# Kernel tuning notes

Measured on AMD Instinct MI355X. Metric: run time of the kernel, lower is better.

Reference implementation:

```python
import jax, jax.numpy as jnp
import numpy as np

N_NODES = 100000
N_EDGES = 800000
NODE_F = 32
EDGE_F = 16
HID = 128
EPS = 1e-5


def _bn(h, g, b):
    # BatchNorm1d in training mode: biased batch stats over dim 0
    m = h.mean(axis=0)
    v = jnp.mean((h - m) ** 2, axis=0)
    return (h - m) * jax.lax.rsqrt(v + EPS) * g + b


def _sage(x, src, dst, Wl, bl, Wr):
    # PyG SAGEConv (mean aggr): lin_l(mean_{j->i} x_j) + lin_r(x_i)
    s = jax.ops.segment_sum(x[src], dst, num_segments=N_NODES)
    cnt = jax.ops.segment_sum(jnp.ones((src.shape[0], 1), x.dtype), dst, num_segments=N_NODES)
    mean = s / jnp.maximum(cnt, 1.0)
    return mean @ Wl + bl + x @ Wr


def setup_inputs() -> dict:
    key = jax.random.key(0)
    ks = jax.random.split(key, 32)

    def lin(k, fi, fo):
        return jax.random.normal(k, (fi, fo), jnp.float32) / np.sqrt(fi)

    inp = {
        'x': jax.random.normal(ks[0], (N_NODES, NODE_F), jnp.float32),
        'edge_index': jax.random.randint(ks[1], (2, N_EDGES), 0, N_NODES),
        'edge_attr': jax.random.normal(ks[2], (N_EDGES, EDGE_F), jnp.float32),
        'edge_source': jax.random.randint(ks[3], (N_EDGES,), 0, N_NODES),
        'edge_target': jax.random.randint(ks[4], (N_EDGES,), 0, N_NODES),
        'W1l': lin(ks[5], NODE_F, HID), 'b1': jnp.zeros((HID,), jnp.float32), 'W1r': lin(ks[6], NODE_F, HID),
        'W2l': lin(ks[7], HID, HID), 'b2': jnp.zeros((HID,), jnp.float32), 'W2r': lin(ks[8], HID, HID),
        'bn1_g': jnp.ones((HID,), jnp.float32), 'bn1_b': jnp.zeros((HID,), jnp.float32),
        'bn2_g': jnp.ones((HID,), jnp.float32), 'bn2_b': jnp.zeros((HID,), jnp.float32),
        'We': lin(ks[9], EDGE_F, HID), 'be': jnp.zeros((HID,), jnp.float32),
        'bne_g': jnp.ones((HID,), jnp.float32), 'bne_b': jnp.zeros((HID,), jnp.float32),
        'Wm1': lin(ks[10], 3 * HID, HID), 'bm1': jnp.zeros((HID,), jnp.float32),
        'bnm_g': jnp.ones((HID,), jnp.float32), 'bnm_b': jnp.zeros((HID,), jnp.float32),
        'Wm2': lin(ks[11], HID, HID // 2), 'bm2': jnp.zeros((HID // 2,), jnp.float32),
        'Wm3': lin(ks[12], HID // 2, 1), 'bm3': jnp.zeros((1,), jnp.float32),
    }
    return inp


def reference(x, edge_index, edge_attr, edge_source, edge_target,
              W1l, b1, W1r, W2l, b2, W2r, bn1_g, bn1_b, bn2_g, bn2_b,
              We, be, bne_g, bne_b, Wm1, bm1, bnm_g, bnm_b, Wm2, bm2, Wm3, bm3):
    src, dst = edge_index[0], edge_index[1]
    h = jax.nn.relu(_bn(_sage(x, src, dst, W1l, b1, W1r), bn1_g, bn1_b))  # dropout = identity (eval)
    h = jax.nn.relu(_bn(_sage(h, src, dst, W2l, b2, W2r), bn2_g, bn2_b))
    ef = _bn(jax.nn.relu(edge_attr @ We + be), bne_g, bne_b)  # Linear->ReLU->BN->Dropout(id)
    z = jnp.concatenate([h[edge_source], h[edge_target], ef], axis=1)  # [E, 3*HID]
    z = _bn(jax.nn.relu(z @ Wm1 + bm1), bnm_g, bnm_b)
    z = jax.nn.relu(z @ Wm2 + bm2)
    return (z @ Wm3 + bm3).squeeze(-1)
```

## Files before the change

### kernel.cpp

```cpp
#include <hip/hip_runtime.h>
#include <hip/hip_bf16.h>

#define NN 100000
#define NE 800000
#define SCAN_NB 98

typedef __attribute__((ext_vector_type(8))) short bf16x8;
typedef __attribute__((ext_vector_type(4))) float f32x4;

__device__ __forceinline__ short f2b(float f) {
    unsigned u = __float_as_uint(f);
    unsigned r = (u + 0x7fffu + ((u >> 16) & 1u)) >> 16;
    return (short)r;
}
__device__ __forceinline__ float b2f(short s) {
    return __uint_as_float(((unsigned)(unsigned short)s) << 16);
}

__global__ __launch_bounds__(256) void k_hist(const int* __restrict__ ei, int* __restrict__ deg)
{
    int e = blockIdx.x * 256 + threadIdx.x;
    if (e < NE) atomicAdd(&deg[ei[NE + e]], 1);
}

__global__ __launch_bounds__(1024) void k_scan_a(const int* __restrict__ deg,
    int* __restrict__ tmp, int* __restrict__ bsum)
{
    __shared__ int sh[1024];
    int t = threadIdx.x, b = blockIdx.x;
    int idx = b * 1024 + t;
    int v = (idx < NN) ? deg[idx] : 0;
    sh[t] = v;
    __syncthreads();
    for (int ofs = 1; ofs < 1024; ofs <<= 1) {
        int u = (t >= ofs) ? sh[t - ofs] : 0;
        __syncthreads();
        sh[t] += u;
        __syncthreads();
    }
    if (idx < NN) tmp[idx] = sh[t] - v;
    if (t == 1023) bsum[b] = sh[1023];
}

__global__ void k_scan_b(const int* __restrict__ bsum, int* __restrict__ boff,
    int* __restrict__ rowptr)
{
    if (threadIdx.x == 0) {
        int acc = 0;
        for (int i = 0; i < SCAN_NB; i++) { boff[i] = acc; acc += bsum[i]; }
        rowptr[NN] = acc;
    }
}

__global__ __launch_bounds__(1024) void k_scan_c(const int* __restrict__ tmp,
    const int* __restrict__ boff, int* __restrict__ rowptr, int* __restrict__ wp)
{
    int b = blockIdx.x, t = threadIdx.x;
    int idx = b * 1024 + t;
    if (idx < NN) {
        int v = boff[b] + tmp[idx];
        rowptr[idx] = v; wp[idx] = v;
    }
}

__global__ __launch_bounds__(256) void k_scatter(const int* __restrict__ ei,
    int* __restrict__ wp, int* __restrict__ elist)
{
    int e = blockIdx.x * 256 + threadIdx.x;
    if (e < NE) {
        int d = ei[NE + e];
        int pos = atomicAdd(&wp[d], 1);
        elist[pos] = ei[e];
    }
}

__global__ __launch_bounds__(256) void k_gagg1(const float* __restrict__ x,
    const int* __restrict__ rowptr, const int* __restrict__ elist, float* __restrict__ meanX)
{
    int n = blockIdx.x * 8 + (threadIdx.x >> 5);
    int j = threadIdx.x & 31;
    int b = rowptr[n], e = rowptr[n + 1];
    float acc = 0.f;
    for (int i = b; i < e; i++) {
        int s = elist[i];
        acc += x[(size_t)s * 32 + j];
    }
    float inv = (e > b) ? 1.0f / (float)(e - b) : 1.0f;
    meanX[(size_t)n * 32 + j] = acc * inv;
}

__global__ __launch_bounds__(256) void k_gagg2(const short* __restrict__ h1b,
    const int* __restrict__ rowptr, const int* __restrict__ elist,
    const float* __restrict__ ssum, const float* __restrict__ ssq,
    const float* __restrict__ g, const float* __restrict__ bb, short* __restrict__ m2b)
{
    __shared__ float sS[128], sH[128];
    int tid = threadIdx.x;
    if (tid < 128) {
        float m = ssum[tid] / (float)NN;
        float var = ssq[tid] / (float)NN - m * m;
        float rs = rsqrtf(var + 1e-5f);
        float sc = g[tid] * rs;
        sS[tid] = sc; sH[tid] = bb[tid] - m * sc;
    }
    __syncthreads();
    int n = blockIdx.x * 8 + (tid >> 5);
    int c0 = (tid & 31) * 4;
    float sc[4], sh[4];
    #pragma unroll
    for (int i = 0; i < 4; i++) { sc[i] = sS[c0 + i]; sh[i] = sH[c0 + i]; }
    int b = rowptr[n], e = rowptr[n + 1];
    float acc[4] = {0.f, 0.f, 0.f, 0.f};
    for (int i = b; i < e; i++) {
        int s = elist[i];
        ushort4 u = *(const ushort4*)(h1b + (size_t)s * 128 + c0);
        acc[0] += fmaxf(b2f((short)u.x) * sc[0] + sh[0], 0.f);
        acc[1] += fmaxf(b2f((short)u.y) * sc[1] + sh[1], 0.f);
        acc[2] += fmaxf(b2f((short)u.z) * sc[2] + sh[2], 0.f);
        acc[3] += fmaxf(b2f((short)u.w) * sc[3] + sh[3], 0.f);
    }
    float inv = (e > b) ? 1.0f / (float)(e - b) : 1.0f;
    ushort4 o;
    o.x = (unsigned short)f2b(acc[0] * inv);
    o.y = (unsigned short)f2b(acc[1] * inv);
    o.z = (unsigned short)f2b(acc[2] * inv);
    o.w = (unsigned short)f2b(acc[3] * inv);
    *(ushort4*)(m2b + (size_t)n * 128 + c0) = o;
}

__global__ __launch_bounds__(256) void k_node_l1(
    const float* __restrict__ meanX, const float* __restrict__ x,
    const float* __restrict__ Wl, const float* __restrict__ Wr,
    const float* __restrict__ bias,
    short* __restrict__ outp, float* __restrict__ ssum, float* __restrict__ ssq)
{
    __shared__ __align__(16) float sWl[32][128];
    __shared__ __align__(16) float sWr[32][128];
    __shared__ __align__(16) float sA[32][36];
    __shared__ __align__(16) float sB[32][36];
    __shared__ float red[2][128], red2[2][128];
    int tid = threadIdx.x;
    int j = tid & 127, rg = tid >> 7;
    int r0 = blockIdx.x * 32;

    for (int f = tid * 4; f < 4096; f += 1024) {
        *(float4*)((float*)sWl + f) = *(const float4*)(Wl + f);
        *(float4*)((float*)sWr + f) = *(const float4*)(Wr + f);
    }
    {
        int r = tid >> 3, c = (tid & 7) * 4;
        *(float4*)(&sA[r][c]) = *(const float4*)(meanX + (size_t)(r0 + r) * 32 + c);
        *(float4*)(&sB[r][c]) = *(const float4*)(x + (size_t)(r0 + r) * 32 + c);
    }
    __syncthreads();

    float acc[16];
    #pragma unroll
    for (int r = 0; r < 16; r++) acc[r] = 0.0f;
    int rb = rg * 16;
    #pragma unroll
    for (int kq = 0; kq < 8; kq++) {
        int k = kq * 4;
        float wl0 = sWl[k][j], wl1 = sWl[k+1][j], wl2 = sWl[k+2][j], wl3 = sWl[k+3][j];
        float wr0 = sWr[k][j], wr1 = sWr[k+1][j], wr2 = sWr[k+2][j], wr3 = sWr[k+3][j];
        #pragma unroll
        for (int r = 0; r < 16; r++) {
            float4 a = *(float4*)(&sA[rb + r][k]);
            float4 b = *(float4*)(&sB[rb + r][k]);
            acc[r] += a.x*wl0 + a.y*wl1 + a.z*wl2 + a.w*wl3
                    + b.x*wr0 + b.y*wr1 + b.z*wr2 + b.w*wr3;
        }
    }
    float bj = bias[j];
    float s1 = 0.0f, s2 = 0.0f;
    #pragma unroll
    for (int r = 0; r < 16; r++) {
        float v = acc[r] + bj;
        outp[(size_t)(r0 + rb + r) * 128 + j] = f2b(v);
        s1 += v; s2 += v * v;
    }
    red[rg][j] = s1; red2[rg][j] = s2;
    __syncthreads();
    if (rg == 0) {
        atomicAdd(&ssum[j], red[0][j] + red[1][j]);
        atomicAdd(&ssq[j],  red2[0][j] + red2[1][j]);
    }
}

__global__ __launch_bounds__(256) void k_node_l2m(
    const short* __restrict__ m2b, const short* __restrict__ h1b,
    const float* __restrict__ s1sum, const float* __restrict__ s1sq,
    const float* __restrict__ g1, const float* __restrict__ b1b,
    const short* __restrict__ W2cT, const float* __restrict__ bias,
    short* __restrict__ h2b, float* __restrict__ ssum, float* __restrict__ ssq)
{
    __shared__ __align__(16) short sK[32][264];
    __shared__ float sRed[2][128];
    __shared__ float sS[128], sH[128];
    const int tid = threadIdx.x;
    const int wave = tid >> 6, lane = tid & 63, quad = lane >> 4, ln = lane & 15;
    const int waveM = wave >> 1, waveN = wave & 1;
    const int colbase = 64 * waveN, row16 = 16 * waveM;
    if (tid < 128) {
        float m = s1sum[tid] / (float)NN;
        float var = s1sq[tid] / (float)NN - m * m;
        float rs = rsqrtf(var + 1e-5f);
        float sc = g1[tid] * rs;
        sS[tid] = sc; sH[tid] = b1b[tid] - m * sc;
        sRed[0][tid] = 0.f; sRed[1][tid] = 0.f;
    }

    bf16x8 bW[4][8];
    #pragma unroll
    for (int nt = 0; nt < 4; nt++)
        #pragma unroll
        for (int kk = 0; kk < 8; kk++)
            bW[nt][kk] = *(const bf16x8*)(W2cT + (size_t)(colbase + nt * 16 + ln) * 256 + kk * 32 + quad * 8);
    float bc[4];
    #pragma unroll
    for (int nt = 0; nt < 4; nt++) bc[nt] = bias[colbase + nt * 16 + ln];

    float s1[4] = {0,0,0,0}, s2[4] = {0,0,0,0};
    f32x4 zero = {0.f, 0.f, 0.f, 0.f};
    __syncthreads();

    for (int t = blockIdx.x; t < NN / 32; t += gridDim.x) {
        int r0 = t * 32;
        __syncthreads();
        {
            int r = tid >> 3, seg = tid & 7;
            if (seg < 4) {
                const bf16x8* src = (const bf16x8*)(m2b + (size_t)(r0 + r) * 128 + seg * 32);
                bf16x8* dst = (bf16x8*)(&sK[r][seg * 32]);
                dst[0] = src[0]; dst[1] = src[1]; dst[2] = src[2]; dst[3] = src[3];
            } else {
                int c0 = (seg - 4) * 32;
                const short* src = h1b + (size_t)(r0 + r) * 128 + c0;
                short tmp[32];
                #pragma unroll
                for (int i = 0; i < 32; i++)
                    tmp[i] = f2b(fmaxf(b2f(src[i]) * sS[c0 + i] + sH[c0 + i], 0.f));
                bf16x8* dst = (bf16x8*)(&sK[r][128 + c0]);
                dst[0] = *(bf16x8*)(tmp); dst[1] = *(bf16x8*)(tmp + 8);
                dst[2] = *(bf16x8*)(tmp + 16); dst[3] = *(bf16x8*)(tmp + 24);
            }
        }
        __syncthreads();
        f32x4 acc[4] = {zero, zero, zero, zero};
        #pragma unroll
        for (int kk = 0; kk < 8; kk++) {
            bf16x8 a = *(const bf16x8*)(&sK[row16 + ln][kk * 32 + quad * 8]);
            #pragma unroll
            for (int nt = 0; nt < 4; nt++)
                acc[nt] = __builtin_amdgcn_mfma_f32_16x16x32_bf16(a, bW[nt][kk], acc[nt], 0, 0, 0);
        }
        #pragma unroll
        for (int nt = 0; nt < 4; nt++) {
            int col = colbase + nt * 16 + ln;
            #pragma unroll
            for (int r = 0; r < 4; r++) {
                float v = acc[nt][r] + bc[nt];
                h2b[(size_t)(r0 + row16 + quad * 4 + r) * 128 + col] = f2b(v);
                s1[nt] += v; s2[nt] += v * v;
            }
        }
    }
    #pragma unroll
    for (int nt = 0; nt < 4; nt++) {
        float a1 = s1[nt], a2 = s2[nt];
        a1 += __shfl_down(a1, 32); a1 += __shfl_down(a1, 16);
        a2 += __shfl_down(a2, 32); a2 += __shfl_down(a2, 16);
        if (quad == 0) {
            atomicAdd(&sRed[0][colbase + nt * 16 + ln], a1);
            atomicAdd(&sRed[1][colbase + nt * 16 + ln], a2);
        }
    }
    __syncthreads();
    if (tid < 128) {
        atomicAdd(&ssum[tid], sRed[0][tid]);
        atomicAdd(&ssq[tid],  sRed[1][tid]);
    }
}

__global__ void k_prep(const float* __restrict__ We, const float* __restrict__ Wm1,
                       const float* __restrict__ W2l, const float* __restrict__ W2r,
                       short* __restrict__ WteT, short* __restrict__ WmsT,
                       short* __restrict__ WmdT, short* __restrict__ W2cT)
{
    int j = threadIdx.x;
    int b = blockIdx.x;
    if (b == 0) {
        for (int k = 0; k < 32; k++)
            WteT[j * 32 + k] = (k < 16) ? f2b(We[k * 128 + j]) : (short)0;
    } else if (b == 1) {
        for (int k = 0; k < 128; k++) WmsT[j * 128 + k] = f2b(Wm1[k * 128 + j]);
    } else if (b == 2) {
        for (int k = 0; k < 128; k++) WmdT[j * 128 + k] = f2b(Wm1[(128 + k) * 128 + j]);
    } else if (b == 3) {
        for (int k = 0; k < 128; k++) W2cT[j * 256 + k] = f2b(W2l[k * 128 + j]);
    } else {
        for (int k = 0; k < 128; k++) W2cT[j * 256 + 128 + k] = f2b(W2r[k * 128 + j]);
    }
}

__global__ void k_fold_e(const float* __restrict__ ssum, const float* __restrict__ ssq,
    const float* __restrict__ g, const float* __restrict__ b,
    const float* __restrict__ Wm1, const float* __restrict__ bm1,
    short* __restrict__ W1pT, float* __restrict__ bm1p)
{
    __shared__ float sa[128], sc[128];
    int tid = threadIdx.x;
    float m = ssum[tid] / (float)NE;
    float var = ssq[tid] / (float)NE - m * m;
    float rs = rsqrtf(var + 1e-5f);
    float a = g[tid] * rs;
    sa[tid] = a; sc[tid] = b[tid] - m * a;
    __syncthreads();
    float acc = bm1[tid];
    for (int k = 0; k < 128; k++) {
        float w = Wm1[(256 + k) * 128 + tid];
        W1pT[tid * 128 + k] = f2b(sa[k] * w);
        acc += sc[k] * w;
    }
    bm1p[tid] = acc;
}

__global__ void k_fold_m(const float* __restrict__ ssum, const float* __restrict__ ssq,
    const float* __restrict__ g, const float* __restrict__ b,
    const float* __restrict__ Wm2, const float* __restrict__ bm2,
    short* __restrict__ W2pT, float* __restrict__ b2p)
{
    __shared__ float sa[128], sc[128];
    int tid = threadIdx.x;
    float m = ssum[tid] / (float)NE;
    float var = ssq[tid] / (float)NE - m * m;
    float rs = rsqrtf(var + 1e-5f);
    float a = g[tid] * rs;
    sa[tid] = a; sc[tid] = b[tid] - m * a;
    __syncthreads();
    if (tid < 64) {
        float acc = bm2[tid];
        for (int k = 0; k < 128; k++) {
            float w = Wm2[k * 64 + tid];
            W2pT[tid * 128 + k] = f2b(sa[k] * w);
            acc += sc[k] * w;
        }
        b2p[tid] = acc;
    }
}

__global__ __launch_bounds__(256) void k_proj2(
    const short* __restrict__ h2b,
    const float* __restrict__ s2sum, const float* __restrict__ s2sq,
    const float* __restrict__ g2, const float* __restrict__ b2b,
    const short* __restrict__ WsT, const short* __restrict__ WdT,
    short* __restrict__ Cs, short* __restrict__ Cd)
{
    __shared__ __align__(16) short sA[32][136];
    __shared__ float sS[128], sH[128];
    const int tid = threadIdx.x;
    const int wave = tid >> 6, lane = tid & 63, quad = lane >> 4, ln = lane & 15;
    const int waveM = wave >> 1, waveN = wave & 1;
    const int colbase = 64 * waveN, row16 = 16 * waveM;
    if (tid < 128) {
        float m = s2sum[tid] / (float)NN;
        float var = s2sq[tid] / (float)NN - m * m;
        float rs = rsqrtf(var + 1e-5f);
        float sc = g2[tid] * rs;
        sS[tid] = sc; sH[tid] = b2b[tid] - m * sc;
    }
    bf16x8 bWs[4][4], bWd[4][4];
    #pragma unroll
    for (int nt = 0; nt < 4; nt++)
        #pragma unroll
        for (int kk = 0; kk < 4; kk++) {
            bWs[nt][kk] = *(const bf16x8*)(WsT + (colbase + nt * 16 + ln) * 128 + kk * 32 + quad * 8);
            bWd[nt][kk] = *(const bf16x8*)(WdT + (colbase + nt * 16 + ln) * 128 + kk * 32 + quad * 8);
        }
    f32x4 zero = {0.f, 0.f, 0.f, 0.f};
    __syncthreads();
    for (int t = blockIdx.x; t < NN / 32; t += gridDim.x) {
        int r0 = t * 32;
        __syncthreads();
        {
            int r = tid >> 3, c0 = (tid & 7) * 16;
            const short* p = h2b + (size_t)(r0 + r) * 128 + c0;
            short tmp[16];
            #pragma unroll
            for (int i = 0; i < 16; i++)
                tmp[i] = f2b(fmaxf(b2f(p[i]) * sS[c0 + i] + sH[c0 + i], 0.f));
            *(bf16x8*)(&sA[r][c0])     = *(bf16x8*)tmp;
            *(bf16x8*)(&sA[r][c0 + 8]) = *(bf16x8*)(tmp + 8);
        }
        __syncthreads();
        f32x4 accS[4] = {zero, zero, zero, zero};
        f32x4 accD[4] = {zero, zero, zero, zero};
        #pragma unroll
        for (int kk = 0; kk < 4; kk++) {
            bf16x8 a = *(const bf16x8*)(&sA[row16 + ln][kk * 32 + quad * 8]);
            #pragma unroll
            for (int nt = 0; nt < 4; nt++) {
                accS[nt] = __builtin_amdgcn_mfma_f32_16x16x32_bf16(a, bWs[nt][kk], accS[nt], 0, 0, 0);
                accD[nt] = __builtin_amdgcn_mfma_f32_16x16x32_bf16(a, bWd[nt][kk], accD[nt], 0, 0, 0);
            }
        }
        #pragma unroll
        for (int nt = 0; nt < 4; nt++) {
            int col = colbase + nt * 16 + ln;
            #pragma unroll
            for (int r = 0; r < 4; r++) {
                size_t idx = (size_t)(r0 + row16 + quad * 4 + r) * 128 + col;
                Cs[idx] = f2b(accS[nt][r]);
                Cd[idx] = f2b(accD[nt][r]);
            }
        }
    }
}

template<int MODE>
__global__ __launch_bounds__(256) void k_edge_mfma(
    const float* __restrict__ ea, short* __restrict__ ea_bf,
    const short* __restrict__ WteT, const float* __restrict__ be,
    const short* __restrict__ W1pT, const float* __restrict__ bm1p,
    const short* __restrict__ hs, const short* __restrict__ hd,
    const int* __restrict__ esrc, const int* __restrict__ etgt,
    const short* __restrict__ W2pT, const float* __restrict__ b2p,
    const float* __restrict__ Wm3, const float* __restrict__ bm3,
    float* __restrict__ ssum, float* __restrict__ ssq,
    float* __restrict__ outp)
{
    __shared__ __align__(16) short sT[32][136];
    __shared__ float sRed[2][128];
    __shared__ __align__(16) float sG[32][132];
    __shared__ __align__(16) short sW2[64][136];
    __shared__ float sZ[32][69];
    __shared__ float sW3[64];

    const int tid = threadIdx.x;
    const int wave = tid >> 6, lane = tid & 63;
    const int quad = lane >> 4, ln = lane & 15;
    const int waveM = wave >> 1, waveN = wave & 1;
    const int colbase = 64 * waveN, row16 = 16 * waveM;

    if (MODE < 2) {
        if (tid < 128) { sRed[0][tid] = 0.f; sRed[1][tid] = 0.f; }
    }
    if (MODE == 2) {
        int q = tid >> 2, kb = (tid & 3) * 32;
        const bf16x8* src = (const bf16x8*)(W2pT + q * 128 + kb);
        bf16x8* dst = (bf16x8*)(&sW2[q][kb]);
        dst[0] = src[0]; dst[1] = src[1]; dst[2] = src[2]; dst[3] = src[3];
        if (tid < 64) sW3[tid] = Wm3[tid];
    }

    bf16x8 bWe[4], bW1[4][4];
    #pragma unroll
    for (int nt = 0; nt < 4; nt++) {
        bWe[nt] = *(const bf16x8*)(WteT + (colbase + nt * 16 + ln) * 32 + quad * 8);
        if (MODE >= 1) {
            #pragma unroll
            for (int kk = 0; kk < 4; kk++)
                bW1[nt][kk] = *(const bf16x8*)(W1pT + (colbase + nt * 16 + ln) * 128 + kk * 32 + quad * 8);
        }
    }
    float bec[4], bmc[4];
    #pragma unroll
    for (int nt = 0; nt < 4; nt++) {
        bec[nt] = be[colbase + nt * 16 + ln];
        bmc[nt] = (MODE >= 1) ? bm1p[colbase + nt * 16 + ln] : 0.f;
    }
    float b2c[2] = {0.f, 0.f};
    if (MODE == 2) { b2c[0] = b2p[32 * waveN + ln]; b2c[1] = b2p[32 * waveN + 16 + ln]; }
    float bm3v = (MODE == 2) ? bm3[0] : 0.f;

    const int g_er = tid >> 3, g_cb = (tid & 7) * 16;

    float s1[4] = {0,0,0,0}, s2[4] = {0,0,0,0};
    f32x4 zero = {0.f, 0.f, 0.f, 0.f};
    __syncthreads();

    for (int t = blockIdx.x; t < NE / 32; t += gridDim.x) {
        const int e0 = t * 32;

        bf16x8 ga0, ga1, gb0, gb1;
        if (MODE >= 1) {
            int es_ = esrc[e0 + g_er], et_ = etgt[e0 + g_er];
            const short* ps = hs + (size_t)es_ * 128 + g_cb;
            const short* pd = hd + (size_t)et_ * 128 + g_cb;
            ga0 = *(const bf16x8*)ps;      ga1 = *(const bf16x8*)(ps + 8);
            gb0 = *(const bf16x8*)pd;      gb1 = *(const bf16x8*)(pd + 8);
        }

        bf16x8 aE;
        #pragma unroll
        for (int i = 0; i < 8; i++) aE[i] = 0;
        if (MODE == 0) {
            if (quad < 2) {
                const float* p = ea + (size_t)(e0 + row16 + ln) * 16 + quad * 8;
                float4 f0 = *(const float4*)p, f1 = *(const float4*)(p + 4);
                aE[0]=f2b(f0.x); aE[1]=f2b(f0.y); aE[2]=f2b(f0.z); aE[3]=f2b(f0.w);
                aE[4]=f2b(f1.x); aE[5]=f2b(f1.y); aE[6]=f2b(f1.z); aE[7]=f2b(f1.w);
                if (waveN == 0)
                    *(bf16x8*)(ea_bf + (size_t)(e0 + row16 + ln) * 16 + quad * 8) = aE;
            }
        } else {
            if (quad < 2)
                aE = *(const bf16x8*)(ea_bf + (size_t)(e0 + row16 + ln) * 16 + quad * 8);
        }
        f32x4 tacc[4];
        #pragma unroll
        for (int nt = 0; nt < 4; nt++)
            tacc[nt] = __builtin_amdgcn_mfma_f32_16x16x32_bf16(aE, bWe[nt], tacc[nt] = zero, 0, 0, 0);

        if (MODE == 0) {
            #pragma unroll
            for (int nt = 0; nt < 4; nt++)
                #pragma unroll
                for (int r = 0; r < 4; r++) {
                    float v = fmaxf(tacc[nt][r] + bec[nt], 0.f);
                    s1[nt] += v; s2[nt] += v * v;
                }
            continue;
        }

        __syncthreads();
        #pragma unroll
        for (int nt = 0; nt < 4; nt++) {
            int col = colbase + nt * 16 + ln;
            #pragma unroll
            for (int r = 0; r < 4; r++)
                sT[row16 + quad * 4 + r][col] = f2b(fmaxf(tacc[nt][r] + bec[nt], 0.f));
        }
        {
            float tf[16];
            #pragma unroll
            for (int i = 0; i < 8; i++) {
                tf[i]     = b2f(ga0[i]) + b2f(gb0[i]);
                tf[8 + i] = b2f(ga1[i]) + b2f(gb1[i]);
            }
            #pragma unroll
            for (int q4 = 0; q4 < 4; q4++)
                *(float4*)(&sG[g_er][g_cb + q4 * 4]) = *(float4*)(tf + q4 * 4);
        }
        __syncthreads();

        f32x4 uacc[4] = {zero, zero, zero, zero};
        #pragma unroll
        for (int kk = 0; kk < 4; kk++) {
            bf16x8 aU = *(const bf16x8*)(&sT[row16 + ln][kk * 32 + quad * 8]);
            #pragma unroll
            for (int nt = 0; nt < 4; nt++)
                uacc[nt] = __builtin_amdgcn_mfma_f32_16x16x32_bf16(aU, bW1[nt][kk], uacc[nt], 0, 0, 0);
        }

        if (MODE == 1) {
            #pragma unroll
            for (int nt = 0; nt < 4; nt++) {
                int col = colbase + nt * 16 + ln;
                #pragma unroll
                for (int r = 0; r < 4; r++) {
                    float v = uacc[nt][r] + bmc[nt] + sG[row16 + quad * 4 + r][col];
                    v = fmaxf(v, 0.f);
                    s1[nt] += v; s2[nt] += v * v;
                }
            }
        } else {
            __syncthreads();
            #pragma unroll
            for (int nt = 0; nt < 4; nt++) {
                int col = colbase + nt * 16 + ln;
                #pragma unroll
                for (int r = 0; r < 4; r++) {
                    float v = uacc[nt][r] + bmc[nt] + sG[row16 + quad * 4 + r][col];
                    sT[row16 + quad * 4 + r][col] = f2b(fmaxf(v, 0.f));
                }
            }
            __syncthreads();
            f32x4 vacc[2] = {zero, zero};
            #pragma unroll
            for (int kk = 0; kk < 4; kk++) {
                bf16x8 aV = *(const bf16x8*)(&sT[row16 + ln][kk * 32 + quad * 8]);
                #pragma unroll
                for (int n2 = 0; n2 < 2; n2++) {
                    bf16x8 bV = *(const bf16x8*)(&sW2[32 * waveN + n2 * 16 + ln][kk * 32 + quad * 8]);
                    vacc[n2] = __builtin_amdgcn_mfma_f32_16x16x32_bf16(aV, bV, vacc[n2], 0, 0, 0);
                }
            }
            #pragma unroll
            for (int n2 = 0; n2 < 2; n2++) {
                int col2 = 32 * waveN + n2 * 16 + ln;
                #pragma unroll
                for (int r = 0; r < 4; r++)
                    sZ[row16 + quad * 4 + r][col2] = fmaxf(vacc[n2][r] + b2c[n2], 0.f);
            }
            __syncthreads();
            if (wave == 0) {
                int rw = lane & 31, half = lane >> 5;
                float o = 0.f;
                #pragma unroll 8
                for (int k2 = 0; k2 < 32; k2++)
                    o += sZ[rw][half * 32 + k2] * sW3[half * 32 + k2];
                o += __shfl_down(o, 32);
                if (lane < 32) outp[e0 + rw] = o + bm3v;
            }
        }
    }

    if (MODE < 2) {
        #pragma unroll
        for (int nt = 0; nt < 4; nt++) {
            float a1 = s1[nt], a2 = s2[nt];
            a1 += __shfl_down(a1, 32); a1 += __shfl_down(a1, 16);
            a2 += __shfl_down(a2, 32); a2 += __shfl_down(a2, 16);
            if (quad == 0) {
                atomicAdd(&sRed[0][colbase + nt * 16 + ln], a1);
                atomicAdd(&sRed[1][colbase + nt * 16 + ln], a2);
            }
        }
        __syncthreads();
        if (tid < 128) {
            atomicAdd(&ssum[tid], sRed[0][tid]);
            atomicAdd(&ssq[tid],  sRed[1][tid]);
        }
    }
}

extern "C" void kernel_launch(void* const* d_in, const int* in_sizes, int n_in,
                              void* d_out, int out_size, void* d_ws, size_t ws_size,
                              hipStream_t stream) {
    const float* x     = (const float*)d_in[0];
    const int*   ei    = (const int*)  d_in[1];
    const float* eattr = (const float*)d_in[2];
    const int*   esrc  = (const int*)  d_in[3];
    const int*   etgt  = (const int*)  d_in[4];
    const float* W1l = (const float*)d_in[5];  const float* b1 = (const float*)d_in[6];
    const float* W1r = (const float*)d_in[7];
    const float* W2l = (const float*)d_in[8];  const float* b2 = (const float*)d_in[9];
    const float* W2r = (const float*)d_in[10];
    const float* bn1_g = (const float*)d_in[11]; const float* bn1_b = (const float*)d_in[12];
    const float* bn2_g = (const float*)d_in[13]; const float* bn2_b = (const float*)d_in[14];
    const float* We  = (const float*)d_in[15]; const float* be  = (const float*)d_in[16];
    const float* bne_g = (const float*)d_in[17]; const float* bne_b = (const float*)d_in[18];
    const float* Wm1 = (const float*)d_in[19]; const float* bm1 = (const float*)d_in[20];
    const float* bnm_g = (const float*)d_in[21]; const float* bnm_b = (const float*)d_in[22];
    const float* Wm2 = (const float*)d_in[23]; const float* bm2 = (const float*)d_in[24];
    const float* Wm3 = (const float*)d_in[25]; const float* bm3 = (const float*)d_in[26];
    float* out = (float*)d_out;

    char* base = (char*)d_ws;
    size_t o = 0;
    auto A = [&](size_t bytes) { char* p = base + o; o = (o + bytes + 255) & ~(size_t)255; return p; };
    short* hsb   = (short*)A((size_t)NN * 128 * 2);
    short* hdb   = (short*)A((size_t)NN * 128 * 2);
    short* ea_bf = (short*)A((size_t)NE * 16 * 2);
    int*   deg   = (int*)  A((size_t)NN * 4);
    int*   rowptr= (int*)  A((size_t)(NN + 1) * 4);
    int*   wp    = (int*)  A((size_t)NN * 4);
    int*   elist = (int*)  A((size_t)NE * 4);
    float* st    = (float*)A(1024 * 4);
    int*   bsum  = (int*)  A(SCAN_NB * 4);
    int*   boff  = (int*)  A(SCAN_NB * 4);
    float* bm1p  = (float*)A(512); float* b2p = (float*)A(256);
    short* WteT  = (short*)A(128 * 32 * 2);
    short* W1pT  = (short*)A(128 * 128 * 2);
    short* WmsT  = (short*)A(128 * 128 * 2);
    short* WmdT  = (short*)A(128 * 128 * 2);
    short* W2pT  = (short*)A(64 * 128 * 2);
    short* W2cT  = (short*)A(128 * 256 * 2);
    float* meanX = (float*)A((size_t)NN * 32 * 4);
    short* h1b   = (short*)A((size_t)NN * 128 * 2);
    short* m2b   = (short*)A((size_t)NN * 128 * 2);
    short* h2b   = (short*)A((size_t)NN * 128 * 2);
    int*   stmp  = (int*)meanX;

    hipMemsetAsync(deg, 0, (size_t)NN * 4, stream);
    hipMemsetAsync(st, 0, 1024 * 4, stream);

    k_prep<<<5, 128, 0, stream>>>(We, Wm1, W2l, W2r, WteT, WmsT, WmdT, W2cT);
    k_hist<<<(NE + 255) / 256, 256, 0, stream>>>(ei, deg);
    k_scan_a<<<SCAN_NB, 1024, 0, stream>>>(deg, stmp, bsum);
    k_scan_b<<<1, 64, 0, stream>>>(bsum, boff, rowptr);
    k_scan_c<<<SCAN_NB, 1024, 0, stream>>>(stmp, boff, rowptr, wp);
    k_scatter<<<(NE + 255) / 256, 256, 0, stream>>>(ei, wp, elist);

    k_edge_mfma<0><<<1024, 256, 0, stream>>>(eattr, ea_bf, WteT, be, W1pT, bm1p, hsb, hdb,
        esrc, etgt, W2pT, b2p, Wm3, bm3, st + 512, st + 640, out);
    k_fold_e<<<1, 128, 0, stream>>>(st + 512, st + 640, bne_g, bne_b, Wm1, bm1, W1pT, bm1p);

    k_gagg1<<<NN / 8, 256, 0, stream>>>(x, rowptr, elist, meanX);
    k_node_l1<<<NN / 32, 256, 0, stream>>>(meanX, x, W1l, W1r, b1, h1b, st + 0, st + 128);

    k_gagg2<<<NN / 8, 256, 0, stream>>>(h1b, rowptr, elist, st + 0, st + 128, bn1_g, bn1_b, m2b);
    k_node_l2m<<<640, 256, 0, stream>>>(m2b, h1b, st + 0, st + 128, bn1_g, bn1_b,
                                        W2cT, b2, h2b, st + 256, st + 384);

    k_proj2<<<640, 256, 0, stream>>>(h2b, st + 256, st + 384, bn2_g, bn2_b, WmsT, WmdT, hsb, hdb);

    k_edge_mfma<1><<<2048, 256, 0, stream>>>(eattr, ea_bf, WteT, be, W1pT, bm1p, hsb, hdb,
        esrc, etgt, W2pT, b2p, Wm3, bm3, st + 768, st + 896, out);
    k_fold_m<<<1, 128, 0, stream>>>(st + 768, st + 896, bnm_g, bnm_b, Wm2, bm2, W2pT, b2p);

    k_edge_mfma<2><<<2048, 256, 0, stream>>>(eattr, ea_bf, WteT, be, W1pT, bm1p, hsb, hdb,
        esrc, etgt, W2pT, b2p, Wm3, bm3, nullptr, nullptr, out);
}
```

Baseline: 876.7 us.

## Shrink edge kernel LDS via per-mode pool, keep W2 in registers, shuffle final dot

Replaces fixed shared arrays with a per-MODE sized LDS pool so MODE 0 uses almost no LDS and modes 1/2 use less, which allows more resident blocks. W2 tiles are now held in registers instead of being staged in LDS. The final 64-to-1 projection is done with in-wave shuffles instead of an sZ staging buffer read by a single wave. One barrier is dropped in MODE 2. The cost is more VGPRs for the bW2 fragments, and the missing barrier relies on the later barriers to protect reuse of sT and sG across iterations.

```diff
diff --git a/kernel.cpp b/kernel.cpp
--- a/kernel.cpp
+++ b/kernel.cpp
@@ -429,12 +429,12 @@
     float* __restrict__ ssum, float* __restrict__ ssq,
     float* __restrict__ outp)
 {
-    __shared__ __align__(16) short sT[32][136];
-    __shared__ float sRed[2][128];
-    __shared__ __align__(16) float sG[32][132];
-    __shared__ __align__(16) short sW2[64][136];
-    __shared__ float sZ[32][69];
-    __shared__ float sW3[64];
+    constexpr int POOL = (MODE == 0) ? 1024 : (MODE == 1 ? 25600 + 1024 : 25600 + 256);
+    __shared__ __align__(16) char pool[POOL];
+    short (*sT)[136] = (short(*)[136])pool;
+    float (*sG)[132] = (float(*)[132])(pool + 8704);
+    float* sRed = (float*)((MODE == 0) ? (char*)pool : pool + 25600);
+    float (*sP)[32] = (float(*)[32])(pool + 25600);
 
     const int tid = threadIdx.x;
     const int wave = tid >> 6, lane = tid & 63;
@@ -443,14 +443,7 @@
     const int colbase = 64 * waveN, row16 = 16 * waveM;
 
     if (MODE < 2) {
-        if (tid < 128) { sRed[0][tid] = 0.f; sRed[1][tid] = 0.f; }
-    }
-    if (MODE == 2) {
-        int q = tid >> 2, kb = (tid & 3) * 32;
-        const bf16x8* src = (const bf16x8*)(W2pT + q * 128 + kb);
-        bf16x8* dst = (bf16x8*)(&sW2[q][kb]);
-        dst[0] = src[0]; dst[1] = src[1]; dst[2] = src[2]; dst[3] = src[3];
-        if (tid < 64) sW3[tid] = Wm3[tid];
+        if (tid < 128) { sRed[tid] = 0.f; sRed[128 + tid] = 0.f; }
     }
 
     bf16x8 bWe[4], bW1[4][4];
@@ -469,8 +462,19 @@
         bec[nt] = be[colbase + nt * 16 + ln];
         bmc[nt] = (MODE >= 1) ? bm1p[colbase + nt * 16 + ln] : 0.f;
     }
-    float b2c[2] = {0.f, 0.f};
-    if (MODE == 2) { b2c[0] = b2p[32 * waveN + ln]; b2c[1] = b2p[32 * waveN + 16 + ln]; }
+    bf16x8 bW2[2][4];
+    float b2c[2] = {0.f, 0.f}, w3c[2] = {0.f, 0.f};
+    if (MODE == 2) {
+        #pragma unroll
+        for (int n2 = 0; n2 < 2; n2++) {
+            int col2 = 32 * waveN + n2 * 16 + ln;
+            b2c[n2] = b2p[col2];
+            w3c[n2] = Wm3[col2];
+            #pragma unroll
+            for (int kk = 0; kk < 4; kk++)
+                bW2[n2][kk] = *(const bf16x8*)(W2pT + col2 * 128 + kk * 32 + quad * 8);
+        }
+    }
     float bm3v = (MODE == 2) ? bm3[0] : 0.f;
 
     const int g_er = tid >> 3, g_cb = (tid & 7) * 16;
@@ -510,7 +514,7 @@
         f32x4 tacc[4];
         #pragma unroll
         for (int nt = 0; nt < 4; nt++)
-            tacc[nt] = __builtin_amdgcn_mfma_f32_16x16x32_bf16(aE, bWe[nt], tacc[nt] = zero, 0, 0, 0);
+            tacc[nt] = __builtin_amdgcn_mfma_f32_16x16x32_bf16(aE, bWe[nt], zero, 0, 0, 0);
 
         if (MODE == 0) {
             #pragma unroll
@@ -523,7 +527,7 @@
             continue;
         }
 
-        __syncthreads();
+        if (MODE == 1) __syncthreads();
         #pragma unroll
         for (int nt = 0; nt < 4; nt++) {
             int col = colbase + nt * 16 + ln;
@@ -581,28 +585,19 @@
             for (int kk = 0; kk < 4; kk++) {
                 bf16x8 aV = *(const bf16x8*)(&sT[row16 + ln][kk * 32 + quad * 8]);
                 #pragma unroll
-                for (int n2 = 0; n2 < 2; n2++) {
-                    bf16x8 bV = *(const bf16x8*)(&sW2[32 * waveN + n2 * 16 + ln][kk * 32 + quad * 8]);
-                    vacc[n2] = __builtin_amdgcn_mfma_f32_16x16x32_bf16(aV, bV, vacc[n2], 0, 0, 0);
-                }
-            }
-            #pragma unroll
-            for (int n2 = 0; n2 < 2; n2++) {
-                int col2 = 32 * waveN + n2 * 16 + ln;
-                #pragma unroll
-                for (int r = 0; r < 4; r++)
-                    sZ[row16 + quad * 4 + r][col2] = fmaxf(vacc[n2][r] + b2c[n2], 0.f);
+                for (int n2 = 0; n2 < 2; n2++)
+                    vacc[n2] = __builtin_amdgcn_mfma_f32_16x16x32_bf16(aV, bW2[n2][kk], vacc[n2], 0, 0, 0);
+            }
+            #pragma unroll
+            for (int r = 0; r < 4; r++) {
+                float p = fmaxf(vacc[0][r] + b2c[0], 0.f) * w3c[0]
+                        + fmaxf(vacc[1][r] + b2c[1], 0.f) * w3c[1];
+                p += __shfl_xor(p, 1); p += __shfl_xor(p, 2);
+                p += __shfl_xor(p, 4); p += __shfl_xor(p, 8);
+                if (ln == 0) sP[waveN][row16 + quad * 4 + r] = p;
             }
             __syncthreads();
-            if (wave == 0) {
-                int rw = lane & 31, half = lane >> 5;
-                float o = 0.f;
-                #pragma unroll 8
-                for (int k2 = 0; k2 < 32; k2++)
-                    o += sZ[rw][half * 32 + k2] * sW3[half * 32 + k2];
-                o += __shfl_down(o, 32);
-                if (lane < 32) outp[e0 + rw] = o + bm3v;
-            }
+            if (tid < 32) outp[e0 + tid] = sP[0][tid] + sP[1][tid] + bm3v;
         }
     }
 
@@ -613,14 +608,14 @@
             a1 += __shfl_down(a1, 32); a1 += __shfl_down(a1, 16);
             a2 += __shfl_down(a2, 32); a2 += __shfl_down(a2, 16);
             if (quad == 0) {
-                atomicAdd(&sRed[0][colbase + nt * 16 + ln], a1);
-                atomicAdd(&sRed[1][colbase + nt * 16 + ln], a2);
+                atomicAdd(&sRed[colbase + nt * 16 + ln], a1);
+                atomicAdd(&sRed[128 + colbase + nt * 16 + ln], a2);
             }
         }
         __syncthreads();
         if (tid < 128) {
-            atomicAdd(&ssum[tid], sRed[0][tid]);
-            atomicAdd(&ssq[tid],  sRed[1][tid]);
+            atomicAdd(&ssum[tid], sRed[tid]);
+            atomicAdd(&ssq[tid],  sRed[128 + tid]);
         }
     }
 }
```

Result: slower. 912.2 us (+4.0%).

## Store MLP hidden activations to skip recomputation in final edge pass

Applied to the files above, without the earlier changes.

When workspace is large enough, the first MLP edge pass writes the post-ReLU hidden activations as bf16 to a buffer that reuses the node-stage scratch region. A new mode-3 pass then reads them back and runs only the second and third layers, avoiding a second round of endpoint gathers and the first-layer GEMM. The first pass also software-prefetches the next tile's gathered rows, and the source/target projection kernel is split into two launches with half the register weights each. This trades 200MB of extra writes and reads for the recomputation, and it depends on the workspace size.

```diff
diff --git a/kernel.cpp b/kernel.cpp
--- a/kernel.cpp
+++ b/kernel.cpp
@@ -349,12 +349,11 @@
     }
 }
 
-__global__ __launch_bounds__(256) void k_proj2(
+__global__ __launch_bounds__(256) void k_proj_mfma(
     const short* __restrict__ h2b,
     const float* __restrict__ s2sum, const float* __restrict__ s2sq,
     const float* __restrict__ g2, const float* __restrict__ b2b,
-    const short* __restrict__ WsT, const short* __restrict__ WdT,
-    short* __restrict__ Cs, short* __restrict__ Cd)
+    const short* __restrict__ WT, short* __restrict__ C)
 {
     __shared__ __align__(16) short sA[32][136];
     __shared__ float sS[128], sH[128];
@@ -369,14 +368,12 @@
         float sc = g2[tid] * rs;
         sS[tid] = sc; sH[tid] = b2b[tid] - m * sc;
     }
-    bf16x8 bWs[4][4], bWd[4][4];
+    bf16x8 bW[4][4];
     #pragma unroll
     for (int nt = 0; nt < 4; nt++)
         #pragma unroll
-        for (int kk = 0; kk < 4; kk++) {
-            bWs[nt][kk] = *(const bf16x8*)(WsT + (colbase + nt * 16 + ln) * 128 + kk * 32 + quad * 8);
-            bWd[nt][kk] = *(const bf16x8*)(WdT + (colbase + nt * 16 + ln) * 128 + kk * 32 + quad * 8);
-        }
+        for (int kk = 0; kk < 4; kk++)
+            bW[nt][kk] = *(const bf16x8*)(WT + (colbase + nt * 16 + ln) * 128 + kk * 32 + quad * 8);
     f32x4 zero = {0.f, 0.f, 0.f, 0.f};
     __syncthreads();
     for (int t = blockIdx.x; t < NN / 32; t += gridDim.x) {
@@ -393,31 +390,25 @@
             *(bf16x8*)(&sA[r][c0 + 8]) = *(bf16x8*)(tmp + 8);
         }
         __syncthreads();
-        f32x4 accS[4] = {zero, zero, zero, zero};
-        f32x4 accD[4] = {zero, zero, zero, zero};
+        f32x4 acc[4] = {zero, zero, zero, zero};
         #pragma unroll
         for (int kk = 0; kk < 4; kk++) {
             bf16x8 a = *(const bf16x8*)(&sA[row16 + ln][kk * 32 + quad * 8]);
             #pragma unroll
-            for (int nt = 0; nt < 4; nt++) {
-                accS[nt] = __builtin_amdgcn_mfma_f32_16x16x32_bf16(a, bWs[nt][kk], accS[nt], 0, 0, 0);
-                accD[nt] = __builtin_amdgcn_mfma_f32_16x16x32_bf16(a, bWd[nt][kk], accD[nt], 0, 0, 0);
-            }
+            for (int nt = 0; nt < 4; nt++)
+                acc[nt] = __builtin_amdgcn_mfma_f32_16x16x32_bf16(a, bW[nt][kk], acc[nt], 0, 0, 0);
         }
         #pragma unroll
         for (int nt = 0; nt < 4; nt++) {
             int col = colbase + nt * 16 + ln;
             #pragma unroll
-            for (int r = 0; r < 4; r++) {
-                size_t idx = (size_t)(r0 + row16 + quad * 4 + r) * 128 + col;
-                Cs[idx] = f2b(accS[nt][r]);
-                Cd[idx] = f2b(accD[nt][r]);
-            }
-        }
-    }
-}
-
-template<int MODE>
+            for (int r = 0; r < 4; r++)
+                C[(size_t)(r0 + row16 + quad * 4 + r) * 128 + col] = f2b(acc[nt][r]);
+        }
+    }
+}
+
+template<int MODE, bool STOREV = false>
 __global__ __launch_bounds__(256) void k_edge_mfma(
     const float* __restrict__ ea, short* __restrict__ ea_bf,
     const short* __restrict__ WteT, const float* __restrict__ be,
@@ -427,7 +418,7 @@
     const short* __restrict__ W2pT, const float* __restrict__ b2p,
     const float* __restrict__ Wm3, const float* __restrict__ bm3,
     float* __restrict__ ssum, float* __restrict__ ssq,
-    float* __restrict__ outp)
+    short* __restrict__ vbuf, float* __restrict__ outp)
 {
     __shared__ __align__(16) short sT[32][136];
     __shared__ float sRed[2][128];
@@ -445,7 +436,7 @@
     if (MODE < 2) {
         if (tid < 128) { sRed[0][tid] = 0.f; sRed[1][tid] = 0.f; }
     }
-    if (MODE == 2) {
+    if (MODE >= 2) {
         int q = tid >> 2, kb = (tid & 3) * 32;
         const bf16x8* src = (const bf16x8*)(W2pT + q * 128 + kb);
         bf16x8* dst = (bf16x8*)(&sW2[q][kb]);
@@ -454,41 +445,90 @@
     }
 
     bf16x8 bWe[4], bW1[4][4];
+    if (MODE <= 2) {
+        #pragma unroll
+        for (int nt = 0; nt < 4; nt++) {
+            bWe[nt] = *(const bf16x8*)(WteT + (colbase + nt * 16 + ln) * 32 + quad * 8);
+            if (MODE >= 1) {
+                #pragma unroll
+                for (int kk = 0; kk < 4; kk++)
+                    bW1[nt][kk] = *(const bf16x8*)(W1pT + (colbase + nt * 16 + ln) * 128 + kk * 32 + quad * 8);
+            }
+        }
+    }
+    float bec[4], bmc[4];
     #pragma unroll
     for (int nt = 0; nt < 4; nt++) {
-        bWe[nt] = *(const bf16x8*)(WteT + (colbase + nt * 16 + ln) * 32 + quad * 8);
-        if (MODE >= 1) {
-            #pragma unroll
-            for (int kk = 0; kk < 4; kk++)
-                bW1[nt][kk] = *(const bf16x8*)(W1pT + (colbase + nt * 16 + ln) * 128 + kk * 32 + quad * 8);
-        }
-    }
-    float bec[4], bmc[4];
-    #pragma unroll
-    for (int nt = 0; nt < 4; nt++) {
-        bec[nt] = be[colbase + nt * 16 + ln];
-        bmc[nt] = (MODE >= 1) ? bm1p[colbase + nt * 16 + ln] : 0.f;
+        bec[nt] = (MODE <= 2) ? be[colbase + nt * 16 + ln] : 0.f;
+        bmc[nt] = (MODE == 1 || MODE == 2) ? bm1p[colbase + nt * 16 + ln] : 0.f;
     }
     float b2c[2] = {0.f, 0.f};
-    if (MODE == 2) { b2c[0] = b2p[32 * waveN + ln]; b2c[1] = b2p[32 * waveN + 16 + ln]; }
-    float bm3v = (MODE == 2) ? bm3[0] : 0.f;
+    if (MODE >= 2) { b2c[0] = b2p[32 * waveN + ln]; b2c[1] = b2p[32 * waveN + 16 + ln]; }
+    float bm3v = (MODE >= 2) ? bm3[0] : 0.f;
 
     const int g_er = tid >> 3, g_cb = (tid & 7) * 16;
+    const int NT = NE / 32;
+
+    bf16x8 ga0, ga1, gb0, gb1;
+    if (MODE == 1 && blockIdx.x < NT) {
+        int es0 = esrc[blockIdx.x * 32 + g_er], et0 = etgt[blockIdx.x * 32 + g_er];
+        const short* ps = hs + (size_t)es0 * 128 + g_cb;
+        const short* pd = hd + (size_t)et0 * 128 + g_cb;
+        ga0 = *(const bf16x8*)ps; ga1 = *(const bf16x8*)(ps + 8);
+        gb0 = *(const bf16x8*)pd; gb1 = *(const bf16x8*)(pd + 8);
+    }
 
     float s1[4] = {0,0,0,0}, s2[4] = {0,0,0,0};
     f32x4 zero = {0.f, 0.f, 0.f, 0.f};
     __syncthreads();
 
-    for (int t = blockIdx.x; t < NE / 32; t += gridDim.x) {
+    for (int t = blockIdx.x; t < NT; t += gridDim.x) {
         const int e0 = t * 32;
 
-        bf16x8 ga0, ga1, gb0, gb1;
-        if (MODE >= 1) {
+        if (MODE == 3) {
+            f32x4 vacc[2] = {zero, zero};
+            #pragma unroll
+            for (int kk = 0; kk < 4; kk++) {
+                bf16x8 aV = *(const bf16x8*)(vbuf + (size_t)(e0 + row16 + ln) * 128 + kk * 32 + quad * 8);
+                #pragma unroll
+                for (int n2 = 0; n2 < 2; n2++) {
+                    bf16x8 bV = *(const bf16x8*)(&sW2[32 * waveN + n2 * 16 + ln][kk * 32 + quad * 8]);
+                    vacc[n2] = __builtin_amdgcn_mfma_f32_16x16x32_bf16(aV, bV, vacc[n2], 0, 0, 0);
+                }
+            }
+            __syncthreads();
+            #pragma unroll
+            for (int n2 = 0; n2 < 2; n2++) {
+                int col2 = 32 * waveN + n2 * 16 + ln;
+                #pragma unroll
+                for (int r = 0; r < 4; r++)
+                    sZ[row16 + quad * 4 + r][col2] = fmaxf(vacc[n2][r] + b2c[n2], 0.f);
+            }
+            __syncthreads();
+            if (wave == 0) {
+                int rw = lane & 31, half = lane >> 5;
+                float o = 0.f;
+                #pragma unroll 8
+                for (int k2 = 0; k2 < 32; k2++)
+                    o += sZ[rw][half * 32 + k2] * sW3[half * 32 + k2];
+                o += __shfl_down(o, 32);
+                if (lane < 32) outp[e0 + rw] = o + bm3v;
+            }
+            continue;
+        }
+
+        int tn = t + gridDim.x;
+        int es_n = 0, et_n = 0;
+        if (MODE == 1 && tn < NT) {
+            es_n = esrc[tn * 32 + g_er];
+            et_n = etgt[tn * 32 + g_er];
+        }
+        if (MODE == 2) {
             int es_ = esrc[e0 + g_er], et_ = etgt[e0 + g_er];
             const short* ps = hs + (size_t)es_ * 128 + g_cb;
             const short* pd = hd + (size_t)et_ * 128 + g_cb;
-            ga0 = *(const bf16x8*)ps;      ga1 = *(const bf16x8*)(ps + 8);
-            gb0 = *(const bf16x8*)pd;      gb1 = *(const bf16x8*)(pd + 8);
+            ga0 = *(const bf16x8*)ps; ga1 = *(const bf16x8*)(ps + 8);
+            gb0 = *(const bf16x8*)pd; gb1 = *(const bf16x8*)(pd + 8);
         }
 
         bf16x8 aE;
@@ -510,7 +550,7 @@
         f32x4 tacc[4];
         #pragma unroll
         for (int nt = 0; nt < 4; nt++)
-            tacc[nt] = __builtin_amdgcn_mfma_f32_16x16x32_bf16(aE, bWe[nt], tacc[nt] = zero, 0, 0, 0);
+            tacc[nt] = __builtin_amdgcn_mfma_f32_16x16x32_bf16(aE, bWe[nt], zero, 0, 0, 0);
 
         if (MODE == 0) {
             #pragma unroll
@@ -542,6 +582,13 @@
             for (int q4 = 0; q4 < 4; q4++)
                 *(float4*)(&sG[g_er][g_cb + q4 * 4]) = *(float4*)(tf + q4 * 4);
         }
+        bf16x8 na0 = ga0, na1 = ga1, nb0 = gb0, nb1 = gb1;
+        if (MODE == 1 && tn < NT) {
+            const short* ps = hs + (size_t)es_n * 128 + g_cb;
+            const short* pd = hd + (size_t)et_n * 128 + g_cb;
+            na0 = *(const bf16x8*)ps; na1 = *(const bf16x8*)(ps + 8);
+            nb0 = *(const bf16x8*)pd; nb1 = *(const bf16x8*)(pd + 8);
+        }
         __syncthreads();
 
         f32x4 uacc[4] = {zero, zero, zero, zero};
@@ -554,16 +601,35 @@
         }
 
         if (MODE == 1) {
-            #pragma unroll
-            for (int nt = 0; nt < 4; nt++) {
-                int col = colbase + nt * 16 + ln;
-                #pragma unroll
-                for (int r = 0; r < 4; r++) {
-                    float v = uacc[nt][r] + bmc[nt] + sG[row16 + quad * 4 + r][col];
-                    v = fmaxf(v, 0.f);
-                    s1[nt] += v; s2[nt] += v * v;
+            if constexpr (STOREV) {
+                __syncthreads();
+                #pragma unroll
+                for (int nt = 0; nt < 4; nt++) {
+                    int col = colbase + nt * 16 + ln;
+                    #pragma unroll
+                    for (int r = 0; r < 4; r++) {
+                        float v = uacc[nt][r] + bmc[nt] + sG[row16 + quad * 4 + r][col];
+                        v = fmaxf(v, 0.f);
+                        s1[nt] += v; s2[nt] += v * v;
+                        sT[row16 + quad * 4 + r][col] = f2b(v);
+                    }
                 }
-            }
+                __syncthreads();
+                *(bf16x8*)(vbuf + (size_t)(e0 + g_er) * 128 + g_cb)     = *(bf16x8*)(&sT[g_er][g_cb]);
+                *(bf16x8*)(vbuf + (size_t)(e0 + g_er) * 128 + g_cb + 8) = *(bf16x8*)(&sT[g_er][g_cb + 8]);
+            } else {
+                #pragma unroll
+                for (int nt = 0; nt < 4; nt++) {
+                    int col = colbase + nt * 16 + ln;
+                    #pragma unroll
+                    for (int r = 0; r < 4; r++) {
+                        float v = uacc[nt][r] + bmc[nt] + sG[row16 + quad * 4 + r][col];
+                        v = fmaxf(v, 0.f);
+                        s1[nt] += v; s2[nt] += v * v;
+                    }
+                }
+            }
+            ga0 = na0; ga1 = na1; gb0 = nb0; gb1 = nb1;
         } else {
             __syncthreads();
             #pragma unroll
@@ -667,11 +733,14 @@
     short* WmdT  = (short*)A(128 * 128 * 2);
     short* W2pT  = (short*)A(64 * 128 * 2);
     short* W2cT  = (short*)A(128 * 256 * 2);
+    size_t chain = o;
     float* meanX = (float*)A((size_t)NN * 32 * 4);
     short* h1b   = (short*)A((size_t)NN * 128 * 2);
     short* m2b   = (short*)A((size_t)NN * 128 * 2);
     short* h2b   = (short*)A((size_t)NN * 128 * 2);
     int*   stmp  = (int*)meanX;
+    short* vbuf  = (short*)(base + chain);
+    bool storev = ws_size >= chain + (size_t)NE * 128 * 2;
 
     hipMemsetAsync(deg, 0, (size_t)NN * 4, stream);
     hipMemsetAsync(st, 0, 1024 * 4, stream);
@@ -684,7 +753,7 @@
     k_scatter<<<(NE + 255) / 256, 256, 0, stream>>>(ei, wp, elist);
 
     k_edge_mfma<0><<<1024, 256, 0, stream>>>(eattr, ea_bf, WteT, be, W1pT, bm1p, hsb, hdb,
-        esrc, etgt, W2pT, b2p, Wm3, bm3, st + 512, st + 640, out);
+        esrc, etgt, W2pT, b2p, Wm3, bm3, st + 512, st + 640, nullptr, out);
     k_fold_e<<<1, 128, 0, stream>>>(st + 512, st + 640, bne_g, bne_b, Wm1, bm1, W1pT, bm1p);
 
     k_gagg1<<<NN / 8, 256, 0, stream>>>(x, rowptr, elist, meanX);
@@ -694,12 +763,21 @@
     k_node_l2m<<<640, 256, 0, stream>>>(m2b, h1b, st + 0, st + 128, bn1_g, bn1_b,
                                         W2cT, b2, h2b, st + 256, st + 384);
 
-    k_proj2<<<640, 256, 0, stream>>>(h2b, st + 256, st + 384, bn2_g, bn2_b, WmsT, WmdT, hsb, hdb);
-
-    k_edge_mfma<1><<<2048, 256, 0, stream>>>(eattr, ea_bf, WteT, be, W1pT, bm1p, hsb, hdb,
-        esrc, etgt, W2pT, b2p, Wm3, bm3, st + 768, st + 896, out);
+    k_proj_mfma<<<640, 256, 0, stream>>>(h2b, st + 256, st + 384, bn2_g, bn2_b, WmsT, hsb);
+    k_proj_mfma<<<640, 256, 0, stream>>>(h2b, st + 256, st + 384, bn2_g, bn2_b, WmdT, hdb);
+
+    if (storev)
+        k_edge_mfma<1, true><<<2048, 256, 0, stream>>>(eattr, ea_bf, WteT, be, W1pT, bm1p, hsb, hdb,
+            esrc, etgt, W2pT, b2p, Wm3, bm3, st + 768, st + 896, vbuf, out);
+    else
+        k_edge_mfma<1, false><<<2048, 256, 0, stream>>>(eattr, ea_bf, WteT, be, W1pT, bm1p, hsb, hdb,
+            esrc, etgt, W2pT, b2p, Wm3, bm3, st + 768, st + 896, nullptr, out);
     k_fold_m<<<1, 128, 0, stream>>>(st + 768, st + 896, bnm_g, bnm_b, Wm2, bm2, W2pT, b2p);
 
-    k_edge_mfma<2><<<2048, 256, 0, stream>>>(eattr, ea_bf, WteT, be, W1pT, bm1p, hsb, hdb,
-        esrc, etgt, W2pT, b2p, Wm3, bm3, nullptr, nullptr, out);
-}
+    if (storev)
+        k_edge_mfma<3><<<2048, 256, 0, stream>>>(eattr, ea_bf, WteT, be, W1pT, bm1p, hsb, hdb,
+            esrc, etgt, W2pT, b2p, Wm3, bm3, nullptr, nullptr, vbuf, out);
+    else
+        k_edge_mfma<2><<<2048, 256, 0, stream>>>(eattr, ea_bf, WteT, be, W1pT, bm1p, hsb, hdb,
+            esrc, etgt, W2pT, b2p, Wm3, bm3, nullptr, nullptr, nullptr, out);
+}
```

Result: slower. 894.8 us (+2.1%).
